# Optimization experiments

Measured on AMD Instinct MI355X. Metric: run time of the kernel, lower is better.

## Reference

```python
import jax, jax.numpy as jnp
import numpy as np

D, H, DH = 768, 12, 64
W = 256            # one-sided window (attention_window=512 total)
EPS = 1e-6
NEG = -1e9


def layer_norm(x, g, b):
    m = jnp.mean(x, axis=-1, keepdims=True)
    v = jnp.mean((x - m) ** 2, axis=-1, keepdims=True)
    return g * (x - m) * jax.lax.rsqrt(v + EPS) + b


def _blocks3(t, nb):
    # t: [B,H,nb,W,dh] -> keys/values of 3 neighboring blocks [B,H,nb,3W,dh]
    tp = jnp.pad(t, ((0, 0), (0, 0), (1, 1), (0, 0), (0, 0)))
    return jnp.concatenate([tp[:, :, :nb], tp[:, :, 1:nb + 1], tp[:, :, 2:nb + 2]], axis=3)


def sliding_window_attention(x, kpm, Wq, bq, Wk, bk, Wv, bv, Wo, bo):
    B, S, _ = x.shape
    nb = S // W
    def proj(Wm, bm):
        return (x @ Wm + bm).reshape(B, S, H, DH).transpose(0, 2, 1, 3).reshape(B, H, nb, W, DH)
    q = proj(Wq, bq) * (1.0 / np.sqrt(DH))
    k = proj(Wk, bk)
    v = proj(Wv, bv)
    k3 = _blocks3(k, nb)
    v3 = _blocks3(v, nb)
    # scores over local band: [B,H,nb,W,3W]
    s = jnp.einsum('bhnqd,bhnkd->bhnqk', q, k3)
    qi = jnp.arange(W)[:, None]
    kj = jnp.arange(3 * W)[None, :]
    band = jnp.abs(kj - W - qi) <= W                     # [W,3W]
    kg = (jnp.arange(nb)[:, None, None] - 1) * W + kj[None]  # global key idx [nb,1,3W]
    inrange = (kg >= 0) & (kg < S)
    # key padding mask gathered into block layout: [B,nb,3W]
    kpm_b = jnp.pad(kpm.reshape(B, nb, W), ((0, 0), (1, 1), (0, 0)), constant_values=True)
    kpm3 = jnp.concatenate([kpm_b[:, :nb], kpm_b[:, 1:nb + 1], kpm_b[:, 2:nb + 2]], axis=2)
    m = band[None, None, None] & inrange[None, None] & (~kpm3)[:, None, :, None, :]
    s = jnp.where(m, s, NEG)
    p = jax.nn.softmax(s, axis=-1)
    o = jnp.einsum('bhnqk,bhnkd->bhnqd', p, v3)
    o = o.reshape(B, H, S, DH).transpose(0, 2, 1, 3).reshape(B, S, D)
    return o @ Wo + bo


def setup_inputs() -> dict:
    key = jax.random.key(0)
    ks = jax.random.split(key, 12)
    B, S, DF = 2, 4096, 3072
    sc = 1.0 / np.sqrt(D)
    return {
        'x': jax.random.normal(ks[0], (B, S, D), jnp.float32),
        'mask': jnp.zeros((B, S), bool),
        'id': 0,
        'Wq': jax.random.normal(ks[1], (D, D), jnp.float32) * sc,
        'bq': jnp.zeros((D,), jnp.float32),
        'Wk': jax.random.normal(ks[2], (D, D), jnp.float32) * sc,
        'bk': jnp.zeros((D,), jnp.float32),
        'Wv': jax.random.normal(ks[3], (D, D), jnp.float32) * sc,
        'bv': jnp.zeros((D,), jnp.float32),
        'Wo': jax.random.normal(ks[4], (D, D), jnp.float32) * sc,
        'bo': jnp.zeros((D,), jnp.float32),
        'ln1_g': jnp.ones((D,), jnp.float32),
        'ln1_b': jnp.zeros((D,), jnp.float32),
        'W1': jax.random.normal(ks[5], (D, DF), jnp.float32) * sc,
        'b1': jnp.zeros((DF,), jnp.float32),
        'W2': jax.random.normal(ks[6], (DF, D), jnp.float32) * (1.0 / np.sqrt(DF)),
        'b2': jnp.zeros((D,), jnp.float32),
        'ln2_g': jnp.ones((D,), jnp.float32),
        'ln2_b': jnp.zeros((D,), jnp.float32),
    }


def reference(x, mask, id, Wq, bq, Wk, bk, Wv, bv, Wo, bo, ln1_g, ln1_b, W1, b1, W2, b2, ln2_g, ln2_b):
    # Sublayer 1: pre-norm residual around sliding-window self-attention
    h = layer_norm(x, ln1_g, ln1_b)
    x = x + sliding_window_attention(h, mask, Wq, bq, Wk, bk, Wv, bv, Wo, bo)
    # Sublayer 2: pre-norm residual around positionwise FFN
    h = layer_norm(x, ln2_g, ln2_b)
    x = x + (jax.nn.relu(h @ W1 + b1) @ W2 + b2)
    return x
```

## Files before the change

kernel.cpp:

```cpp
#include <hip/hip_runtime.h>
#include <hip/hip_bf16.h>
#include <cstddef>

typedef __attribute__((ext_vector_type(8))) short short8;
typedef __attribute__((ext_vector_type(4))) float f32x4;
typedef __attribute__((ext_vector_type(4))) unsigned short us4;

typedef __attribute__((address_space(1))) void as1_void;
typedef __attribute__((address_space(3))) void as3_void;

__device__ __forceinline__ void gload16(const void* g, void* lds) {
  __builtin_amdgcn_global_load_lds((as1_void*)(void*)g, (as3_void*)lds, 16, 0, 0);
}

__device__ inline unsigned short f2bf(float f) {
  union { float f; unsigned int u; } v; v.f = f;
  return (unsigned short)((v.u + 0x7FFFu + ((v.u >> 16) & 1u)) >> 16);
}

__device__ __forceinline__ float exp2v(float x) {
  float r; asm("v_exp_f32 %0, %1" : "=v"(r) : "v"(x)); return r;
}
__device__ __forceinline__ unsigned cvtpk(float a, float b) {
  unsigned r; asm("v_cvt_pk_bf16_f32 %0, %1, %2" : "=v"(r) : "v"(a), "v"(b)); return r;
}

__global__ __launch_bounds__(256) void ln_kernel(const float* __restrict__ x,
    const float* __restrict__ g, const float* __restrict__ b,
    unsigned short* __restrict__ out)
{
  int row = blockIdx.x, t = threadIdx.x;
  const float* xr = x + (size_t)row * 768;
  float v0 = xr[t], v1 = xr[t + 256], v2 = xr[t + 512];
  float s = v0 + v1 + v2;
  #pragma unroll
  for (int o = 32; o > 0; o >>= 1) s += __shfl_xor(s, o);
  __shared__ float r1[4], r2[4];
  if ((t & 63) == 0) r1[t >> 6] = s;
  __syncthreads();
  float mean = (r1[0] + r1[1] + r1[2] + r1[3]) * (1.0f / 768.0f);
  float d0 = v0 - mean, d1 = v1 - mean, d2 = v2 - mean;
  float q = d0 * d0 + d1 * d1 + d2 * d2;
  #pragma unroll
  for (int o = 32; o > 0; o >>= 1) q += __shfl_xor(q, o);
  if ((t & 63) == 0) r2[t >> 6] = q;
  __syncthreads();
  float var = (r2[0] + r2[1] + r2[2] + r2[3]) * (1.0f / 768.0f);
  float rs = rsqrtf(var + 1e-6f);
  unsigned short* orow = out + (size_t)row * 768;
  orow[t]       = f2bf(g[t]       * d0 * rs + b[t]);
  orow[t + 256] = f2bf(g[t + 256] * d1 * rs + b[t + 256]);
  orow[t + 512] = f2bf(g[t + 512] * d2 * rs + b[t + 512]);
}

__global__ __launch_bounds__(256) void prep_kernel(
    const float* __restrict__ Wq, const float* __restrict__ Wk,
    const float* __restrict__ Wv, const float* __restrict__ Wo,
    const float* __restrict__ W1, const float* __restrict__ W2,
    const float* __restrict__ bq, const float* __restrict__ bk,
    const float* __restrict__ bv,
    unsigned short* __restrict__ WTqkv, unsigned short* __restrict__ WTo,
    unsigned short* __restrict__ W1T, unsigned short* __restrict__ W2T,
    float* __restrict__ bqkv,
    const float* __restrict__ x, const float* __restrict__ ln1g,
    const float* __restrict__ ln1b, unsigned short* __restrict__ hbuf)
{
  int bid = blockIdx.x;
  int t = threadIdx.x;
  if (bid >= 6921) {
    int row = bid - 6921;
    const float* xr = x + (size_t)row * 768;
    float v0 = xr[t], v1 = xr[t + 256], v2 = xr[t + 512];
    float s = v0 + v1 + v2;
    #pragma unroll
    for (int o = 32; o > 0; o >>= 1) s += __shfl_xor(s, o);
    __shared__ float r1[4], r2[4];
    if ((t & 63) == 0) r1[t >> 6] = s;
    __syncthreads();
    float mean = (r1[0] + r1[1] + r1[2] + r1[3]) * (1.0f / 768.0f);
    float d0 = v0 - mean, d1 = v1 - mean, d2 = v2 - mean;
    float q = d0 * d0 + d1 * d1 + d2 * d2;
    #pragma unroll
    for (int o = 32; o > 0; o >>= 1) q += __shfl_xor(q, o);
    if ((t & 63) == 0) r2[t >> 6] = q;
    __syncthreads();
    float var = (r2[0] + r2[1] + r2[2] + r2[3]) * (1.0f / 768.0f);
    float rs = rsqrtf(var + 1e-6f);
    unsigned short* orow = hbuf + (size_t)row * 768;
    orow[t]       = f2bf(ln1g[t]       * d0 * rs + ln1b[t]);
    orow[t + 256] = f2bf(ln1g[t + 256] * d1 * rs + ln1b[t + 256]);
    orow[t + 512] = f2bf(ln1g[t + 512] * d2 * rs + ln1b[t + 512]);
    return;
  }
  if (bid >= 6912) {
    int i = (bid - 6912) * 256 + t;
    bqkv[i] = (i < 768) ? bq[i] : ((i < 1536) ? bk[i - 768] : bv[i - 1536]);
    return;
  }
  const float* W; unsigned short* WT; int K, N, lb;
  if (bid < 576)       { W = Wq; WT = WTqkv;                        K = 768;  N = 768;  lb = bid; }
  else if (bid < 1152) { W = Wk; WT = WTqkv + (size_t)768 * 768;    K = 768;  N = 768;  lb = bid - 576; }
  else if (bid < 1728) { W = Wv; WT = WTqkv + (size_t)1536 * 768;   K = 768;  N = 768;  lb = bid - 1152; }
  else if (bid < 2304) { W = Wo; WT = WTo;                          K = 768;  N = 768;  lb = bid - 1728; }
  else if (bid < 4608) { W = W1; WT = W1T;                          K = 768;  N = 3072; lb = bid - 2304; }
  else                 { W = W2; WT = W2T;                          K = 3072; N = 768;  lb = bid - 4608; }
  int ntN = N >> 5;
  int k0 = (lb / ntN) * 32, n0 = (lb % ntN) * 32;
  __shared__ float tile[32][33];
  int tx = t & 31, ty = t >> 5;
  #pragma unroll
  for (int i = 0; i < 32; i += 8)
    tile[ty + i][tx] = W[(size_t)(k0 + ty + i) * N + n0 + tx];
  __syncthreads();
  #pragma unroll
  for (int i = 0; i < 32; i += 8)
    WT[(size_t)(n0 + ty + i) * K + k0 + tx] = f2bf(tile[tx][ty + i]);
}

enum { EPI_QKV = 0, EPI_RELU = 1, EPI_RESID = 2 };

template<int EPI>
__global__ __launch_bounds__(256) void gemmS_kernel(
    const unsigned short* __restrict__ A, const unsigned short* __restrict__ BT,
    const float* __restrict__ bias, const float* __restrict__ resid,
    void* __restrict__ outp, int M, int N, int K, int ntn)
{
  __shared__ char lds_a[16384];
  __shared__ char lds_b[16384];
  int tid = threadIdx.x;
  int nwg = gridDim.x;
  int bid = ((int)blockIdx.x & 7) * (nwg >> 3) + ((int)blockIdx.x >> 3);
  int mt = bid / ntn, nt = bid % ntn;
  int m0 = mt * 128, n0 = nt * 128;
  int w = tid >> 6, l = tid & 63;
  int wr = w >> 1, wc = w & 1;
  int fr = l & 15, fq = l >> 4;
  int rb = tid >> 3;
  int sw8 = ((tid & 7) ^ (rb & 7)) * 8;
  const unsigned short* As = A  + (size_t)(m0 + rb) * K + sw8;
  const unsigned short* Bs = BT + (size_t)(n0 + rb) * K + sw8;

  f32x4 acc[4][4] = {};
  int NT = K >> 6;
  for (int t = 0; t < NT; ++t) {
    {
      char* dA = lds_a + tid * 16;
      char* dB = lds_b + tid * 16;
      int ko = t * 64;
      #pragma unroll
      for (int c = 0; c < 4; c++) {
        gload16(As + (size_t)(c * 32) * K + ko, dA + c * 4096);
        gload16(Bs + (size_t)(c * 32) * K + ko, dB + c * 4096);
      }
    }
    asm volatile("s_waitcnt vmcnt(0)" ::: "memory");
    __syncthreads();
    #pragma unroll
    for (int h = 0; h < 2; h++) {
      short8 af[4], bf[4];
      int colb = (h * 64 + fq * 16) ^ ((fr & 7) << 4);
      #pragma unroll
      for (int i = 0; i < 4; i++)
        af[i] = *(const short8*)(lds_a + (wr * 64 + i * 16 + fr) * 128 + colb);
      #pragma unroll
      for (int j = 0; j < 4; j++)
        bf[j] = *(const short8*)(lds_b + (wc * 64 + j * 16 + fr) * 128 + colb);
      __builtin_amdgcn_s_setprio(1);
      #pragma unroll
      for (int i = 0; i < 4; i++)
        #pragma unroll
        for (int j = 0; j < 4; j++)
          acc[i][j] = __builtin_amdgcn_mfma_f32_16x16x32_bf16(af[i], bf[j], acc[i][j], 0, 0, 0);
      __builtin_amdgcn_s_setprio(0);
    }
    __syncthreads();
  }

  #pragma unroll
  for (int nj = 0; nj < 4; nj++) {
    int col = n0 + wc * 64 + nj * 16 + fr;
    float bs = bias[col];
    if (EPI == EPI_QKV) {
      int which = (col >= 1536) ? 2 : ((col >= 768) ? 1 : 0);
      int c2 = col - which * 768;
      int hh = c2 >> 6, dh = c2 & 63;
      if (which == 2) {
        unsigned short* dstv = reinterpret_cast<unsigned short*>(outp) + (size_t)2 * 8192 * 768;
        #pragma unroll
        for (int i = 0; i < 4; i++) {
          int row0 = m0 + wr * 64 + i * 16 + fq * 4;
          int bb = row0 >> 12, sl = row0 & 4095;
          us4 pv;
          #pragma unroll
          for (int r = 0; r < 4; r++) pv[r] = f2bf(acc[i][nj][r] + bs);
          *reinterpret_cast<us4*>(&dstv[((size_t)(bb * 12 + hh) * 64 + dh) * 4096 + sl]) = pv;
        }
      } else {
        unsigned short* dst = reinterpret_cast<unsigned short*>(outp) + (size_t)which * 8192 * 768;
        #pragma unroll
        for (int i = 0; i < 4; i++) {
          #pragma unroll
          for (int r = 0; r < 4; r++) {
            int row = m0 + wr * 64 + i * 16 + fq * 4 + r;
            float c = acc[i][nj][r] + bs;
            if (which == 0) c *= 0.18033688011112042f;
            int bb = row >> 12, sl = row & 4095;
            dst[(((size_t)(bb * 12 + hh)) * 4096 + sl) * 64 + dh] = f2bf(c);
          }
        }
      }
    } else if (EPI == EPI_RELU) {
      #pragma unroll
      for (int i = 0; i < 4; i++)
        #pragma unroll
        for (int r = 0; r < 4; r++) {
          int row = m0 + wr * 64 + i * 16 + fq * 4 + r;
          float c = fmaxf(acc[i][nj][r] + bs, 0.0f);
          reinterpret_cast<unsigned short*>(outp)[(size_t)row * N + col] = f2bf(c);
        }
    } else {
      #pragma unroll
      for (int i = 0; i < 4; i++)
        #pragma unroll
        for (int r = 0; r < 4; r++) {
          int row = m0 + wr * 64 + i * 16 + fq * 4 + r;
          float c = acc[i][nj][r] + bs + resid[(size_t)row * N + col];
          reinterpret_cast<float*>(outp)[(size_t)row * N + col] = c;
        }
    }
  }
}

template<int EPI>
__global__ __launch_bounds__(256, 3) void gemmN_kernel(
    const unsigned short* __restrict__ A, const unsigned short* __restrict__ BT,
    const float* __restrict__ bias, const float* __restrict__ resid,
    void* __restrict__ outp, int M, int N, int K, int ntn)
{
  __shared__ char lds[2][24576];
  int tid = threadIdx.x;
  int nwg = gridDim.x;
  int bid = ((int)blockIdx.x & 7) * (nwg >> 3) + ((int)blockIdx.x >> 3);
  int mt = bid / ntn, nt = bid % ntn;
  int m0 = mt * 64, n0 = nt * 128;
  int w = tid >> 6, l = tid & 63;
  int fr = l & 15, fq = l >> 4;
  int rb = tid >> 3;
  int sw8 = ((tid & 7) ^ (rb & 7)) * 8;
  const unsigned short* As = A  + (size_t)(m0 + rb) * K + sw8;
  const unsigned short* Bs = BT + (size_t)(n0 + rb) * K + sw8;

  auto stage = [&](int buf, int kt) {
    char* d = &lds[buf][0] + tid * 16;
    int ko = kt * 64;
    #pragma unroll
    for (int c = 0; c < 2; c++)
      gload16(As + (size_t)(c * 32) * K + ko, d + c * 4096);
    #pragma unroll
    for (int c = 0; c < 4; c++)
      gload16(Bs + (size_t)(c * 32) * K + ko, d + 8192 + c * 4096);
  };

  f32x4 acc[4][2] = {};
  stage(0, 0);
  asm volatile("s_waitcnt vmcnt(0)" ::: "memory");
  __syncthreads();

  int NT = K >> 6;
  for (int t = 0; t < NT; ++t) {
    int R = t & 1;
    if (t + 1 < NT) stage(R ^ 1, t + 1);
    #pragma unroll
    for (int h = 0; h < 2; h++) {
      short8 af[4], bf[2];
      const char* base = &lds[R][0];
      int colb = (h * 64 + fq * 16) ^ ((fr & 7) << 4);
      #pragma unroll
      for (int i = 0; i < 4; i++)
        af[i] = *(const short8*)(base + (i * 16 + fr) * 128 + colb);
      #pragma unroll
      for (int j = 0; j < 2; j++)
        bf[j] = *(const short8*)(base + 8192 + (w * 32 + j * 16 + fr) * 128 + colb);
      __builtin_amdgcn_s_setprio(1);
      #pragma unroll
      for (int i = 0; i < 4; i++)
        #pragma unroll
        for (int j = 0; j < 2; j++)
          acc[i][j] = __builtin_amdgcn_mfma_f32_16x16x32_bf16(af[i], bf[j], acc[i][j], 0, 0, 0);
      __builtin_amdgcn_s_setprio(0);
    }
    asm volatile("s_waitcnt vmcnt(0)" ::: "memory");
    __syncthreads();
  }

  #pragma unroll
  for (int nj = 0; nj < 2; nj++) {
    int col = n0 + w * 32 + nj * 16 + fr;
    float bs = bias[col];
    if (EPI == EPI_RELU) {
      #pragma unroll
      for (int i = 0; i < 4; i++)
        #pragma unroll
        for (int r = 0; r < 4; r++) {
          int row = m0 + i * 16 + fq * 4 + r;
          float c = fmaxf(acc[i][nj][r] + bs, 0.0f);
          reinterpret_cast<unsigned short*>(outp)[(size_t)row * N + col] = f2bf(c);
        }
    } else {
      #pragma unroll
      for (int i = 0; i < 4; i++)
        #pragma unroll
        for (int r = 0; r < 4; r++) {
          int row = m0 + i * 16 + fq * 4 + r;
          float c = acc[i][nj][r] + bs + resid[(size_t)row * N + col];
          reinterpret_cast<float*>(outp)[(size_t)row * N + col] = c;
        }
    }
  }
}

__global__ __launch_bounds__(256) void attn_fused_kernel(
    const unsigned short* __restrict__ qg, const unsigned short* __restrict__ kg,
    const unsigned short* __restrict__ vtg, const unsigned char* __restrict__ kpm,
    unsigned short* __restrict__ attn_out)
{
  __shared__ unsigned short lds_k[3][64 * 64];
  __shared__ unsigned short lds_vt[3][64 * 64];
  __shared__ unsigned short lds_p[4][32 * 64];
  int bid0 = blockIdx.x;
  int bid = (bid0 & 7) * 96 + (bid0 >> 3);
  int qblk = bid & 31, h = (bid >> 5) % 12, b = bid / 384;
  int bh = b * 12 + h;
  int q0 = qblk * 128;
  int tid = threadIdx.x, w = tid >> 6, l = tid & 63;
  int fr = l & 15, fq = l >> 4;
  int qw0 = q0 + w * 32;
  int swzb = (((l & 7) ^ (l >> 3)) << 4);
  const char* qbase  = (const char*)(qg  + (size_t)bh * 4096 * 64);
  const char* kbase  = (const char*)(kg  + (size_t)bh * 4096 * 64);
  const char* vtbase = (const char*)(vtg + (size_t)bh * 64 * 4096);
  const unsigned char* kpmb = kpm + (size_t)b * 4096;

  #pragma unroll
  for (int s = 0; s < 4; s++) {
    int row = w * 32 + s * 8 + (l >> 3);
    gload16(qbase + (size_t)(q0 + row) * 128 + swzb, (char*)lds_p[w] + s * 1024);
  }

  auto stageKVc = [&](int c, int buf) {
    int g0 = q0 - 256 + c * 64;
    g0 = (g0 < 0) ? 0 : ((g0 > 4032) ? 4032 : g0);
    #pragma unroll
    for (int s = 0; s < 2; s++) {
      int row = w * 16 + s * 8 + (l >> 3);
      gload16(kbase + (size_t)(g0 + row) * 128 + swzb,
              (char*)lds_k[buf] + (w * 2 + s) * 1024);
      gload16(vtbase + ((size_t)row * 4096 + g0) * 2 + swzb,
              (char*)lds_vt[buf] + (w * 2 + s) * 1024);
    }
  };

  stageKVc(0, 0);
  stageKVc(1, 1);
  asm volatile("s_waitcnt vmcnt(8)" ::: "memory");

  short8 qf[2][2];
  #pragma unroll
  for (int i = 0; i < 2; i++)
    #pragma unroll
    for (int ks = 0; ks < 2; ks++)
      qf[i][ks] = *(const short8*)((const char*)lds_p[w] + (i * 16 + fr) * 128 +
                    ((ks * 64 + fq * 16) ^ ((fr & 7) << 4)));

  short8 ones;
  #pragma unroll
  for (int e = 0; e < 8; e++) ones[e] = (short)0x3F80;

  f32x4 acc_o[2][4] = {};
  f32x4 acc_l[2] = {};
  float m_st[2] = {-3.0e38f, -3.0e38f};

  for (int c = 0; c < 10; c++) {
    if (c < 9) { asm volatile("s_waitcnt vmcnt(4)" ::: "memory"); }
    else       { asm volatile("s_waitcnt vmcnt(0)" ::: "memory"); }
    __builtin_amdgcn_s_barrier();
    if (c < 8) stageKVc(c + 2, (c + 2) % 3);
    int g0 = q0 - 256 + c * 64;
    bool valid = (g0 >= 0) && (g0 < 4096);
    if (valid) {
      int buf = c % 3;
      unsigned int km[4];
      #pragma unroll
      for (int j = 0; j < 4; j++)
        km[j] = *(const unsigned int*)(kpmb + g0 + 16 * j + 4 * fq);
      bool anyk = __any((km[0] | km[1] | km[2] | km[3]) != 0);
      int rel = g0 - qw0;
      bool edge = anyk || (rel < -225) || (rel > 193);
      short8 kf[4][2];
      #pragma unroll
      for (int j = 0; j < 4; j++)
        #pragma unroll
        for (int ks = 0; ks < 2; ks++)
          kf[j][ks] = *(const short8*)((const char*)lds_k[buf] + (j * 16 + fr) * 128 +
                        ((ks * 64 + fq * 16) ^ ((fr & 7) << 4)));
      f32x4 accs[4][2] = {};
      __builtin_amdgcn_s_setprio(1);
      #pragma unroll
      for (int j = 0; j < 4; j++)
        #pragma unroll
        for (int i = 0; i < 2; i++)
          #pragma unroll
          for (int ks = 0; ks < 2; ks++)
            accs[j][i] = __builtin_amdgcn_mfma_f32_16x16x32_bf16(kf[j][ks], qf[i][ks], accs[j][i], 0, 0, 0);
      __builtin_amdgcn_s_setprio(0);
      #pragma unroll
      for (int i = 0; i < 2; i++) {
        float sv[4][4];
        #pragma unroll
        for (int j = 0; j < 4; j++)
          #pragma unroll
          for (int r = 0; r < 4; r++)
            sv[j][r] = accs[j][i][r];
        if (edge) {
          int base = rel + 4 * fq - fr - 16 * i;
          #pragma unroll
          for (int j = 0; j < 4; j++)
            #pragma unroll
            for (int r = 0; r < 4; r++) {
              int d = base + 16 * j + r;
              bool ok = (d >= -256) && (d <= 256) && (((km[j] >> (8 * r)) & 255u) == 0u);
              if (!ok) sv[j][r] = -1.0e9f;
            }
        }
        float mj[4];
        #pragma unroll
        for (int j = 0; j < 4; j++)
          mj[j] = fmaxf(fmaxf(sv[j][0], sv[j][1]), fmaxf(sv[j][2], sv[j][3]));
        float mv = fmaxf(fmaxf(mj[0], mj[1]), fmaxf(mj[2], mj[3]));
        mv = fmaxf(mv, __shfl_xor(mv, 16));
        mv = fmaxf(mv, __shfl_xor(mv, 32));
        float mo = m_st[i];
        if (!__all(mv - mo <= 8.0f)) {
          float mn = fmaxf(mo, mv);
          float scl = exp2v(mo - mn);
          m_st[i] = mn;
          #pragma unroll
          for (int r = 0; r < 4; r++) {
            float so = __shfl(scl, (l & 48) | ((l >> 2) & 12) | r);
            acc_l[i][r] *= so;
            #pragma unroll
            for (int jd = 0; jd < 4; jd++) acc_o[i][jd][r] *= so;
          }
        }
        float mn = m_st[i];
        char* prow = (char*)lds_p[w] + (i * 16 + fr) * 128;
        #pragma unroll
        for (int j = 0; j < 4; j++) {
          float p0 = exp2v(sv[j][0] - mn), p1 = exp2v(sv[j][1] - mn);
          float p2 = exp2v(sv[j][2] - mn), p3 = exp2v(sv[j][3] - mn);
          uint2 u; u.x = cvtpk(p0, p1); u.y = cvtpk(p2, p3);
          *(uint2*)(prow + ((32 * j + 8 * fq) ^ ((fr & 7) << 4))) = u;
        }
      }
      short8 pf[2][2];
      #pragma unroll
      for (int i = 0; i < 2; i++)
        #pragma unroll
        for (int ks = 0; ks < 2; ks++)
          pf[i][ks] = *(const short8*)((const char*)lds_p[w] + (i * 16 + fr) * 128 +
                        ((ks * 64 + fq * 16) ^ ((fr & 7) << 4)));
      short8 vf[4][2];
      #pragma unroll
      for (int jd = 0; jd < 4; jd++)
        #pragma unroll
        for (int ks = 0; ks < 2; ks++)
          vf[jd][ks] = *(const short8*)((const char*)lds_vt[buf] + (jd * 16 + fr) * 128 +
                        ((ks * 64 + fq * 16) ^ ((fr & 7) << 4)));
      __builtin_amdgcn_s_setprio(1);
      #pragma unroll
      for (int i = 0; i < 2; i++) {
        #pragma unroll
        for (int jd = 0; jd < 4; jd++)
          #pragma unroll
          for (int ks = 0; ks < 2; ks++)
            acc_o[i][jd] = __builtin_amdgcn_mfma_f32_16x16x32_bf16(pf[i][ks], vf[jd][ks], acc_o[i][jd], 0, 0, 0);
        #pragma unroll
        for (int ks = 0; ks < 2; ks++)
          acc_l[i] = __builtin_amdgcn_mfma_f32_16x16x32_bf16(pf[i][ks], ones, acc_l[i], 0, 0, 0);
      }
      __builtin_amdgcn_s_setprio(0);
    }
  }
  #pragma unroll
  for (int i = 0; i < 2; i++) {
    #pragma unroll
    for (int r = 0; r < 4; r++) {
      float inv = 1.0f / acc_l[i][r];
      int qrow = qw0 + i * 16 + fq * 4 + r;
      size_t orow = ((size_t)b * 4096 + qrow) * 768 + h * 64;
      #pragma unroll
      for (int jd = 0; jd < 4; jd++)
        attn_out[orow + jd * 16 + fr] = f2bf(acc_o[i][jd][r] * inv);
    }
  }
}

extern "C" void kernel_launch(void* const* d_in, const int* in_sizes, int n_in,
                              void* d_out, int out_size, void* d_ws, size_t ws_size,
                              hipStream_t stream) {
  const float* x            = (const float*)d_in[0];
  const unsigned char* mask = (const unsigned char*)d_in[1];
  const float* Wq  = (const float*)d_in[3];
  const float* bq  = (const float*)d_in[4];
  const float* Wk  = (const float*)d_in[5];
  const float* bk  = (const float*)d_in[6];
  const float* Wv  = (const float*)d_in[7];
  const float* bv  = (const float*)d_in[8];
  const float* Wo  = (const float*)d_in[9];
  const float* bo  = (const float*)d_in[10];
  const float* ln1g = (const float*)d_in[11];
  const float* ln1b = (const float*)d_in[12];
  const float* W1  = (const float*)d_in[13];
  const float* b1  = (const float*)d_in[14];
  const float* W2  = (const float*)d_in[15];
  const float* b2  = (const float*)d_in[16];
  const float* ln2g = (const float*)d_in[17];
  const float* ln2b = (const float*)d_in[18];
  float* out = (float*)d_out;

  char* ws = (char*)d_ws;
  size_t off = 0;
  auto alloc = [&](size_t bytes) -> void* {
    void* p = ws + off;
    off += (bytes + 255) & ~(size_t)255;
    return p;
  };
  unsigned short* WTqkv = (unsigned short*)alloc((size_t)2304 * 768 * 2);
  unsigned short* WTo   = (unsigned short*)alloc((size_t)768 * 768 * 2);
  unsigned short* W1T   = (unsigned short*)alloc((size_t)3072 * 768 * 2);
  unsigned short* W2T   = (unsigned short*)alloc((size_t)768 * 3072 * 2);
  float*          bqkv  = (float*)alloc(2304 * 4);
  unsigned short* hbuf  = (unsigned short*)alloc((size_t)8192 * 768 * 2);
  unsigned short* qkv   = (unsigned short*)alloc((size_t)3 * 8192 * 768 * 2);
  unsigned short* attn  = (unsigned short*)alloc((size_t)8192 * 768 * 2);
  float* x1             = (float*)alloc((size_t)8192 * 768 * 4);
  unsigned short* h2    = (unsigned short*)alloc((size_t)8192 * 768 * 2);
  unsigned short* a1    = (unsigned short*)alloc((size_t)8192 * 3072 * 2);

  prep_kernel<<<15113, 256, 0, stream>>>(Wq, Wk, Wv, Wo, W1, W2, bq, bk, bv,
                                         WTqkv, WTo, W1T, W2T, bqkv,
                                         x, ln1g, ln1b, hbuf);

  gemmS_kernel<EPI_QKV><<<1152, 256, 0, stream>>>(hbuf, WTqkv, bqkv, nullptr, qkv, 8192, 2304, 768, 18);

  attn_fused_kernel<<<768, 256, 0, stream>>>(qkv, qkv + (size_t)8192 * 768,
                                             qkv + (size_t)2 * 8192 * 768, mask, attn);

  gemmN_kernel<EPI_RESID><<<768, 256, 0, stream>>>(attn, WTo, bo, x, x1, 8192, 768, 768, 6);
  ln_kernel<<<8192, 256, 0, stream>>>(x1, ln2g, ln2b, h2);
  gemmS_kernel<EPI_RELU><<<1536, 256, 0, stream>>>(h2, W1T, b1, nullptr, a1, 8192, 3072, 768, 24);
  gemmN_kernel<EPI_RESID><<<768, 256, 0, stream>>>(a1, W2T, b2, x1, out, 8192, 768, 3072, 6);
}
```

Measured before the change: 232.2 us.

## Enlarge GEMM tiles to 256x128 and double-buffer attention K/V staging

The QKV and FFN1 GEMMs now use 256x128 tiles. Each wave owns 64 rows across all 128 columns, which doubles the accumulators and halves the grid size. B-tile reuse per load goes up, at the cost of more registers and LDS and fewer workgroups (576 and 768). Separately, the attention kernel drops from triple to double buffering of K/V chunks and adds a second barrier per iteration. That cuts LDS use but exposes more load latency.

```diff
diff --git a/kernel.cpp b/kernel.cpp
--- a/kernel.cpp
+++ b/kernel.cpp
@@ -120,27 +120,26 @@
 enum { EPI_QKV = 0, EPI_RELU = 1, EPI_RESID = 2 };
 
 template<int EPI>
-__global__ __launch_bounds__(256) void gemmS_kernel(
+__global__ __launch_bounds__(256) void gemmB_kernel(
     const unsigned short* __restrict__ A, const unsigned short* __restrict__ BT,
-    const float* __restrict__ bias, const float* __restrict__ resid,
-    void* __restrict__ outp, int M, int N, int K, int ntn)
+    const float* __restrict__ bias, void* __restrict__ outp,
+    int M, int N, int K, int ntn)
 {
-  __shared__ char lds_a[16384];
+  __shared__ char lds_a[32768];
   __shared__ char lds_b[16384];
   int tid = threadIdx.x;
   int nwg = gridDim.x;
   int bid = ((int)blockIdx.x & 7) * (nwg >> 3) + ((int)blockIdx.x >> 3);
   int mt = bid / ntn, nt = bid % ntn;
-  int m0 = mt * 128, n0 = nt * 128;
+  int m0 = mt * 256, n0 = nt * 128;
   int w = tid >> 6, l = tid & 63;
-  int wr = w >> 1, wc = w & 1;
   int fr = l & 15, fq = l >> 4;
   int rb = tid >> 3;
   int sw8 = ((tid & 7) ^ (rb & 7)) * 8;
   const unsigned short* As = A  + (size_t)(m0 + rb) * K + sw8;
   const unsigned short* Bs = BT + (size_t)(n0 + rb) * K + sw8;
 
-  f32x4 acc[4][4] = {};
+  f32x4 acc[4][8] = {};
   int NT = K >> 6;
   for (int t = 0; t < NT; ++t) {
     {
@@ -148,28 +147,29 @@
       char* dB = lds_b + tid * 16;
       int ko = t * 64;
       #pragma unroll
-      for (int c = 0; c < 4; c++) {
+      for (int c = 0; c < 8; c++)
         gload16(As + (size_t)(c * 32) * K + ko, dA + c * 4096);
+      #pragma unroll
+      for (int c = 0; c < 4; c++)
         gload16(Bs + (size_t)(c * 32) * K + ko, dB + c * 4096);
-      }
     }
     asm volatile("s_waitcnt vmcnt(0)" ::: "memory");
     __syncthreads();
     #pragma unroll
     for (int h = 0; h < 2; h++) {
-      short8 af[4], bf[4];
+      short8 af[4], bf[8];
       int colb = (h * 64 + fq * 16) ^ ((fr & 7) << 4);
       #pragma unroll
       for (int i = 0; i < 4; i++)
-        af[i] = *(const short8*)(lds_a + (wr * 64 + i * 16 + fr) * 128 + colb);
-      #pragma unroll
-      for (int j = 0; j < 4; j++)
-        bf[j] = *(const short8*)(lds_b + (wc * 64 + j * 16 + fr) * 128 + colb);
+        af[i] = *(const short8*)(lds_a + (w * 64 + i * 16 + fr) * 128 + colb);
+      #pragma unroll
+      for (int j = 0; j < 8; j++)
+        bf[j] = *(const short8*)(lds_b + (j * 16 + fr) * 128 + colb);
       __builtin_amdgcn_s_setprio(1);
       #pragma unroll
       for (int i = 0; i < 4; i++)
         #pragma unroll
-        for (int j = 0; j < 4; j++)
+        for (int j = 0; j < 8; j++)
           acc[i][j] = __builtin_amdgcn_mfma_f32_16x16x32_bf16(af[i], bf[j], acc[i][j], 0, 0, 0);
       __builtin_amdgcn_s_setprio(0);
     }
@@ -177,8 +177,8 @@
   }
 
   #pragma unroll
-  for (int nj = 0; nj < 4; nj++) {
-    int col = n0 + wc * 64 + nj * 16 + fr;
+  for (int nj = 0; nj < 8; nj++) {
+    int col = n0 + nj * 16 + fr;
     float bs = bias[col];
     if (EPI == EPI_QKV) {
       int which = (col >= 1536) ? 2 : ((col >= 768) ? 1 : 0);
@@ -188,7 +188,7 @@
         unsigned short* dstv = reinterpret_cast<unsigned short*>(outp) + (size_t)2 * 8192 * 768;
         #pragma unroll
         for (int i = 0; i < 4; i++) {
-          int row0 = m0 + wr * 64 + i * 16 + fq * 4;
+          int row0 = m0 + w * 64 + i * 16 + fq * 4;
           int bb = row0 >> 12, sl = row0 & 4095;
           us4 pv;
           #pragma unroll
@@ -201,7 +201,7 @@
         for (int i = 0; i < 4; i++) {
           #pragma unroll
           for (int r = 0; r < 4; r++) {
-            int row = m0 + wr * 64 + i * 16 + fq * 4 + r;
+            int row = m0 + w * 64 + i * 16 + fq * 4 + r;
             float c = acc[i][nj][r] + bs;
             if (which == 0) c *= 0.18033688011112042f;
             int bb = row >> 12, sl = row & 4095;
@@ -209,23 +209,14 @@
           }
         }
       }
-    } else if (EPI == EPI_RELU) {
+    } else {
       #pragma unroll
       for (int i = 0; i < 4; i++)
         #pragma unroll
         for (int r = 0; r < 4; r++) {
-          int row = m0 + wr * 64 + i * 16 + fq * 4 + r;
+          int row = m0 + w * 64 + i * 16 + fq * 4 + r;
           float c = fmaxf(acc[i][nj][r] + bs, 0.0f);
           reinterpret_cast<unsigned short*>(outp)[(size_t)row * N + col] = f2bf(c);
-        }
-    } else {
-      #pragma unroll
-      for (int i = 0; i < 4; i++)
-        #pragma unroll
-        for (int r = 0; r < 4; r++) {
-          int row = m0 + wr * 64 + i * 16 + fq * 4 + r;
-          float c = acc[i][nj][r] + bs + resid[(size_t)row * N + col];
-          reinterpret_cast<float*>(outp)[(size_t)row * N + col] = c;
         }
     }
   }
@@ -324,8 +315,8 @@
     const unsigned short* __restrict__ vtg, const unsigned char* __restrict__ kpm,
     unsigned short* __restrict__ attn_out)
 {
-  __shared__ unsigned short lds_k[3][64 * 64];
-  __shared__ unsigned short lds_vt[3][64 * 64];
+  __shared__ unsigned short lds_k[2][64 * 64];
+  __shared__ unsigned short lds_vt[2][64 * 64];
   __shared__ unsigned short lds_p[4][32 * 64];
   int bid0 = blockIdx.x;
   int bid = (bid0 & 7) * 96 + (bid0 >> 3);
@@ -361,8 +352,7 @@
   };
 
   stageKVc(0, 0);
-  stageKVc(1, 1);
-  asm volatile("s_waitcnt vmcnt(8)" ::: "memory");
+  asm volatile("s_waitcnt vmcnt(4)" ::: "memory");
 
   short8 qf[2][2];
   #pragma unroll
@@ -381,14 +371,18 @@
   float m_st[2] = {-3.0e38f, -3.0e38f};
 
   for (int c = 0; c < 10; c++) {
-    if (c < 9) { asm volatile("s_waitcnt vmcnt(4)" ::: "memory"); }
-    else       { asm volatile("s_waitcnt vmcnt(0)" ::: "memory"); }
     __builtin_amdgcn_s_barrier();
-    if (c < 8) stageKVc(c + 2, (c + 2) % 3);
+    if (c < 9) {
+      stageKVc(c + 1, (c + 1) & 1);
+      asm volatile("s_waitcnt vmcnt(4)" ::: "memory");
+    } else {
+      asm volatile("s_waitcnt vmcnt(0)" ::: "memory");
+    }
+    __builtin_amdgcn_s_barrier();
     int g0 = q0 - 256 + c * 64;
     bool valid = (g0 >= 0) && (g0 < 4096);
     if (valid) {
-      int buf = c % 3;
+      int buf = c & 1;
       unsigned int km[4];
       #pragma unroll
       for (int j = 0; j < 4; j++)
@@ -551,13 +545,13 @@
                                          WTqkv, WTo, W1T, W2T, bqkv,
                                          x, ln1g, ln1b, hbuf);
 
-  gemmS_kernel<EPI_QKV><<<1152, 256, 0, stream>>>(hbuf, WTqkv, bqkv, nullptr, qkv, 8192, 2304, 768, 18);
+  gemmB_kernel<EPI_QKV><<<576, 256, 0, stream>>>(hbuf, WTqkv, bqkv, qkv, 8192, 2304, 768, 18);
 
   attn_fused_kernel<<<768, 256, 0, stream>>>(qkv, qkv + (size_t)8192 * 768,
                                              qkv + (size_t)2 * 8192 * 768, mask, attn);
 
   gemmN_kernel<EPI_RESID><<<768, 256, 0, stream>>>(attn, WTo, bo, x, x1, 8192, 768, 768, 6);
   ln_kernel<<<8192, 256, 0, stream>>>(x1, ln2g, ln2b, h2);
-  gemmS_kernel<EPI_RELU><<<1536, 256, 0, stream>>>(h2, W1T, b1, nullptr, a1, 8192, 3072, 768, 24);
+  gemmB_kernel<EPI_RELU><<<768, 256, 0, stream>>>(h2, W1T, b1, a1, 8192, 3072, 768, 24);
   gemmN_kernel<EPI_RESID><<<768, 256, 0, stream>>>(a1, W2T, b2, x1, out, 8192, 768, 3072, 6);
 }
```

Measured after the change: 296.4 us. 27.6% more time.
